# Kernel optimization log

Measured on AMD Instinct MI355X. Metric: run time of the kernel, lower is better.

Reference implementation:

```python
import jax, jax.numpy as jnp
import numpy as np

K = 3      # kernel size (fixed by 18 = 2*K*K offset channels)
PAD = 1
EPS = 1e-5 # BatchNorm eps


def setup_inputs() -> dict:
    key = jax.random.key(0)
    ks = jax.random.split(key, 4)
    B, Cin, Cout, H, W = 8, 64, 64, 96, 96
    x = jax.random.normal(ks[0], (B, Cin, H, W), jnp.float32)
    # small offset-conv weights so predicted offsets stay within a few pixels
    w_off = jax.random.normal(ks[1], (2 * K * K, Cin, K, K), jnp.float32) * 0.02
    b_off = jnp.zeros((2 * K * K,), jnp.float32)
    w_def = jax.random.normal(ks[2], (Cout, Cin, K, K), jnp.float32) * (1.0 / np.sqrt(Cin * K * K))
    b_def = jnp.zeros((Cout,), jnp.float32)
    gamma = jnp.ones((Cout,), jnp.float32)
    beta = jnp.zeros((Cout,), jnp.float32)
    return dict(x=x, w_off=w_off, b_off=b_off, w_def=w_def, b_def=b_def, gamma=gamma, beta=beta)


def _deform_sample(x, offset):
    """Bilinear-sample x at deformed kernel tap locations.
    x: (B,C,H,W); offset: (B,2*K*K,H,W) with (dy,dx) pairs per tap, row-major.
    Returns (B,C,K*K,H,W). Out-of-bounds samples are zero (torchvision semantics).
    """
    B, C, H, W = x.shape
    off = offset.reshape(B, K * K, 2, H, W)
    dy, dx = off[:, :, 0], off[:, :, 1]              # (B,9,H,W)
    ky = (jnp.arange(K * K) // K).astype(x.dtype)    # tap row index
    kx = (jnp.arange(K * K) % K).astype(x.dtype)     # tap col index
    base_y = jnp.arange(H, dtype=x.dtype)[:, None] - PAD   # (H,1)
    base_x = jnp.arange(W, dtype=x.dtype)[None, :] - PAD   # (1,W)
    py = dy + ky[None, :, None, None] + base_y[None, None]  # (B,9,H,W)
    px = dx + kx[None, :, None, None] + base_x[None, None]
    y0 = jnp.floor(py)
    x0 = jnp.floor(px)
    wy1 = py - y0
    wx1 = px - x0
    wy0 = 1.0 - wy1
    wx0 = 1.0 - wx1
    xflat = x.reshape(B, C, H * W)
    acc = jnp.zeros((B, C, K * K * H * W), x.dtype)
    corners = [(y0, x0, wy0 * wx0), (y0, x0 + 1.0, wy0 * wx1),
               (y0 + 1.0, x0, wy1 * wx0), (y0 + 1.0, x0 + 1.0, wy1 * wx1)]
    for yc, xc, wc in corners:
        valid = (yc >= 0) & (yc <= H - 1) & (xc >= 0) & (xc <= W - 1)
        iy = jnp.clip(yc, 0, H - 1).astype(jnp.int32)
        ix = jnp.clip(xc, 0, W - 1).astype(jnp.int32)
        idx = (iy * W + ix).reshape(B, 1, K * K * H * W)
        v = jnp.take_along_axis(xflat, idx, axis=2)          # (B,C,9HW) gather
        w = jnp.where(valid, wc, 0.0).reshape(B, 1, K * K * H * W)
        acc = acc + v * w
    return acc.reshape(B, C, K * K, H, W)


def reference(x, w_off, b_off, w_def, b_def, gamma, beta):
    # 1) offset-predicting conv
    offset = jax.lax.conv_general_dilated(
        x, w_off, window_strides=(1, 1), padding=((PAD, PAD), (PAD, PAD)),
        dimension_numbers=("NCHW", "OIHW", "NCHW")) + b_off[None, :, None, None]
    # 2) deformable conv: bilinear gather then per-pixel contraction over (C, taps)
    sampled = _deform_sample(x, offset)                      # (B,C,9,H,W)
    Cout = w_def.shape[0]
    y = jnp.einsum("bckhw,ock->bohw", sampled, w_def.reshape(Cout, -1, K * K))
    y = y + b_def[None, :, None, None]
    # 3) BatchNorm2d (training mode: batch statistics) + ReLU
    mean = y.mean(axis=(0, 2, 3))
    var = y.var(axis=(0, 2, 3))
    y = (y - mean[None, :, None, None]) * jax.lax.rsqrt(var[None, :, None, None] + EPS)
    y = gamma[None, :, None, None] * y + beta[None, :, None, None]
    return jax.nn.relu(y)
```

## Files before the change

kernel.cpp:

```cpp
#include <hip/hip_runtime.h>
#include <hip/hip_bf16.h>
#include <stdint.h>

static constexpr int NBATCH = 8;
static constexpr int Cin  = 64;
static constexpr int Cout = 64;
static constexpr int H = 96, W = 96;
static constexpr int HW   = H * W;
static constexpr int NPIX = NBATCH * HW;
static constexpr int NBLK = NPIX / 64;
static constexpr int BLK_PER_BATCH = HW / 64;
static constexpr float EPS = 1e-5f;

typedef short  bf16x8 __attribute__((ext_vector_type(8)));
typedef float  f32x4  __attribute__((ext_vector_type(4)));

__device__ inline uint16_t f2bf(float f) {
    __hip_bfloat16 h = __float2bfloat16(f);
    return *reinterpret_cast<uint16_t*>(&h);
}
__device__ inline float bf2f(uint16_t u) {
    union { uint32_t i; float f; } z;
    z.i = ((uint32_t)u) << 16;
    return z.f;
}
__device__ inline void gld_lds16(const void* g, void* l) {
    __builtin_amdgcn_global_load_lds(
        (const __attribute__((address_space(1))) void*)g,
        (__attribute__((address_space(3))) void*)l, 16, 0, 0);
}

__global__ void repack(const float* __restrict__ w_off,
                       const float* __restrict__ w_def,
                       uint16_t* __restrict__ woffPack,
                       uint16_t* __restrict__ wdefPack,
                       float* __restrict__ zeropage) {
    int t0 = blockIdx.x * blockDim.x + threadIdx.x;
    int stride = gridDim.x * blockDim.x;
    if (t0 < 64) zeropage[t0] = 0.f;
    for (int i = t0; i < 72 * 32 * 8; i += stride) {
        int e = i & 7;
        int n = (i >> 3) & 31;
        int sg = i >> 8;
        int k = sg * 8 + e;
        int tap = k >> 6, c = k & 63;
        woffPack[i] = (n < 18) ? f2bf(w_off[(n * Cin + c) * 9 + tap]) : (uint16_t)0;
    }
    for (int i = t0; i < 72 * 64 * 8; i += stride) {
        int e = i & 7;
        int n = (i >> 3) & 63;
        int sg = i >> 9;
        int k = sg * 8 + e;
        int tap = k >> 6, c = k & 63;
        wdefPack[i] = f2bf(w_def[(n * Cin + c) * 9 + tap]);
    }
}

__global__ __launch_bounds__(256) void transpose_x(const float* __restrict__ x,
                                                   uint16_t* __restrict__ xT) {
    int t = blockIdx.x * 256 + threadIdx.x;
    int pix  = t >> 1;
    int half = t & 1;
    int b = pix / HW, rem = pix % HW;
    const float* xb = x + (size_t)(b * Cin) * HW + rem + (size_t)(half * 32) * HW;
    uint16_t* o = xT + (size_t)pix * 64 + half * 32;
#pragma unroll
    for (int cg = 0; cg < 4; ++cg) {
        bf16x8 v;
#pragma unroll
        for (int e = 0; e < 8; ++e) v[e] = (short)f2bf(xb[(cg * 8 + e) * HW]);
        *reinterpret_cast<bf16x8*>(o + cg * 8) = v;
    }
}

__global__ __launch_bounds__(512, 4) void fused_deform(
        const uint16_t* __restrict__ xT,
        const uint16_t* __restrict__ woffPack,
        const uint16_t* __restrict__ wdefPack,
        const float* __restrict__ b_off,
        const float* __restrict__ zeropage,
        float* __restrict__ y,
        float* __restrict__ partial) {
    __shared__ __attribute__((aligned(16))) char smem[73728];
    __shared__ float offs[64 * 18];
    __shared__ float s_red[128];
    short* As   = (short*)smem;
    float* osum = (float*)smem;
    float* red  = (float*)smem;

    int tid  = threadIdx.x;
    int lane = tid & 63;
    int wv   = tid >> 6;
    int l15  = lane & 15;
    int lg   = lane >> 4;

    int wgid  = (blockIdx.x & 7) * BLK_PER_BATCH + (blockIdx.x >> 3);
    int gpix0 = wgid * 64;
    int b     = gpix0 / HW;
    int rem0  = gpix0 % HW;
    const uint16_t* xTb = xT + (size_t)b * HW * 64;

    int pr   = (wv << 3) + (lane >> 3);
    int e8   = lane & 7;
    int slot = e8 ^ (pr & 7);
    int remP = rem0 + pr;
    int hP   = remP / W, wP = remP % W;

    {
        const uint16_t* gsrc = xTb + slot * 8;
        char* ldsbase = (char*)As + (size_t)wv * 1024;
#pragma unroll
        for (int tap = 0; tap < 9; ++tap) {
            int yy = hP + tap / 3 - 1;
            int xx = wP + tap % 3 - 1;
            bool ok = (yy >= 0) && (yy < H) && (xx >= 0) && (xx < W);
            const void* g = ok ? (const void*)(gsrc + (yy * W + xx) * 64)
                               : (const void*)zeropage;
            gld_lds16(g, ldsbase + tap * 8192);
        }
    }
    __syncthreads();

    {
        int wj = wv & 1;
        int kq = wv >> 1;
        int sbeg = (kq < 2) ? kq * 5 : 2 + kq * 4;
        int send = (kq < 2) ? sbeg + 5 : sbeg + 4;
        f32x4 oacc[4];
#pragma unroll
        for (int m = 0; m < 4; ++m) oacc[m] = (f32x4){0.f, 0.f, 0.f, 0.f};
        for (int s = sbeg; s < send; ++s) {
            int sg = s * 4 + lg;
            bf16x8 bb = *reinterpret_cast<const bf16x8*>(
                woffPack + (sg * 32 + wj * 16 + l15) * 8);
#pragma unroll
            for (int m = 0; m < 4; ++m) {
                bf16x8 a = *reinterpret_cast<const bf16x8*>(
                    &As[(((sg >> 3) * 64 + m * 16 + l15) * 8 + ((sg & 7) ^ (l15 & 7))) * 8]);
                oacc[m] = __builtin_amdgcn_mfma_f32_16x16x32_bf16(a, bb, oacc[m], 0, 0, 0);
            }
        }
        __syncthreads();
#pragma unroll
        for (int m = 0; m < 4; ++m)
#pragma unroll
            for (int r = 0; r < 4; ++r)
                osum[(kq * 64 + m * 16 + lg * 4 + r) * 34 + wj * 16 + l15] = oacc[m][r];
        __syncthreads();
        for (int i = tid; i < 64 * 18; i += 512) {
            int rr = i / 18, o = i - rr * 18;
            offs[i] = osum[rr * 34 + o] + osum[(64 + rr) * 34 + o]
                    + osum[(128 + rr) * 34 + o] + osum[(192 + rr) * 34 + o] + b_off[o];
        }
        if (tid < 128) s_red[tid] = 0.f;
        __syncthreads();
    }

    {
        float hm1 = (float)(hP - 1), wm1 = (float)(wP - 1);
        float w00a, w01a, w10a, w11a; int i00a, i01a, i10a, i11a;
        {
            int t = e8;
            int ty = (t * 11) >> 5;
            int tx = t - 3 * ty;
            float dy = offs[pr * 18 + 2 * t];
            float dx = offs[pr * 18 + 2 * t + 1];
            float py = dy + (float)ty + hm1;
            float px = dx + (float)tx + wm1;
            float y0f = floorf(py), x0f = floorf(px);
            float wy1 = py - y0f, wx1 = px - x0f;
            float wy0 = 1.f - wy1, wx0 = 1.f - wx1;
            int iy0 = (int)y0f, ix0 = (int)x0f;
            int iy1 = iy0 + 1,  ix1 = ix0 + 1;
            bool vy0 = (iy0 >= 0) && (iy0 < H), vy1 = (iy1 >= 0) && (iy1 < H);
            bool vx0 = (ix0 >= 0) && (ix0 < W), vx1 = (ix1 >= 0) && (ix1 < W);
            w00a = (vy0 && vx0) ? wy0 * wx0 : 0.f;
            w01a = (vy0 && vx1) ? wy0 * wx1 : 0.f;
            w10a = (vy1 && vx0) ? wy1 * wx0 : 0.f;
            w11a = (vy1 && vx1) ? wy1 * wx1 : 0.f;
            int cy0 = min(max(iy0, 0), H - 1), cy1 = min(max(iy1, 0), H - 1);
            int cx0 = min(max(ix0, 0), W - 1), cx1 = min(max(ix1, 0), W - 1);
            i00a = cy0 * W + cx0; i01a = cy0 * W + cx1;
            i10a = cy1 * W + cx0; i11a = cy1 * W + cx1;
        }
        float w00b, w01b, w10b, w11b; int i00b, i01b, i10b, i11b;
        {
            float dy = offs[pr * 18 + 16];
            float dx = offs[pr * 18 + 17];
            float py = dy + 2.f + hm1;
            float px = dx + 2.f + wm1;
            float y0f = floorf(py), x0f = floorf(px);
            float wy1 = py - y0f, wx1 = px - x0f;
            float wy0 = 1.f - wy1, wx0 = 1.f - wx1;
            int iy0 = (int)y0f, ix0 = (int)x0f;
            int iy1 = iy0 + 1,  ix1 = ix0 + 1;
            bool vy0 = (iy0 >= 0) && (iy0 < H), vy1 = (iy1 >= 0) && (iy1 < H);
            bool vx0 = (ix0 >= 0) && (ix0 < W), vx1 = (ix1 >= 0) && (ix1 < W);
            w00b = (vy0 && vx0) ? wy0 * wx0 : 0.f;
            w01b = (vy0 && vx1) ? wy0 * wx1 : 0.f;
            w10b = (vy1 && vx0) ? wy1 * wx0 : 0.f;
            w11b = (vy1 && vx1) ? wy1 * wx1 : 0.f;
            int cy0 = min(max(iy0, 0), H - 1), cy1 = min(max(iy1, 0), H - 1);
            int cx0 = min(max(ix0, 0), W - 1), cx1 = min(max(ix1, 0), W - 1);
            i00b = cy0 * W + cx0; i01b = cy0 * W + cx1;
            i10b = cy1 * W + cx0; i11b = cy1 * W + cx1;
        }

        const uint16_t* basep = xTb + e8 * 8;
        int lanebase = lane & 56;
#pragma unroll
        for (int tap = 0; tap < 9; ++tap) {
            float w00, w01, w10, w11; int i00, i01, i10, i11;
            if (tap < 8) {
                int src = lanebase + tap;
                w00 = __shfl(w00a, src); w01 = __shfl(w01a, src);
                w10 = __shfl(w10a, src); w11 = __shfl(w11a, src);
                i00 = __shfl(i00a, src); i01 = __shfl(i01a, src);
                i10 = __shfl(i10a, src); i11 = __shfl(i11a, src);
            } else {
                w00 = w00b; w01 = w01b; w10 = w10b; w11 = w11b;
                i00 = i00b; i01 = i01b; i10 = i10b; i11 = i11b;
            }
            bf16x8 v00 = *reinterpret_cast<const bf16x8*>(basep + i00 * 64);
            bf16x8 v01 = *reinterpret_cast<const bf16x8*>(basep + i01 * 64);
            bf16x8 v10 = *reinterpret_cast<const bf16x8*>(basep + i10 * 64);
            bf16x8 v11 = *reinterpret_cast<const bf16x8*>(basep + i11 * 64);
            bf16x8 outv;
#pragma unroll
            for (int e = 0; e < 8; ++e) {
                float s = w00 * bf2f((uint16_t)v00[e]) + w01 * bf2f((uint16_t)v01[e])
                        + w10 * bf2f((uint16_t)v10[e]) + w11 * bf2f((uint16_t)v11[e]);
                outv[e] = (short)f2bf(s);
            }
            *reinterpret_cast<bf16x8*>(&As[((tap * 64 + pr) * 8 + slot) * 8]) = outv;
        }
    }
    __syncthreads();

    {
        int nf = wv & 3;
        int kh = wv >> 2;
        f32x4 acc[4];
#pragma unroll
        for (int m = 0; m < 4; ++m) acc[m] = (f32x4){0.f, 0.f, 0.f, 0.f};
#pragma unroll
        for (int s = 0; s < 9; ++s) {
            int sg = (kh * 9 + s) * 4 + lg;
            bf16x8 bb = *reinterpret_cast<const bf16x8*>(
                wdefPack + (sg * 64 + nf * 16 + l15) * 8);
#pragma unroll
            for (int m = 0; m < 4; ++m) {
                bf16x8 a = *reinterpret_cast<const bf16x8*>(
                    &As[(((sg >> 3) * 64 + m * 16 + l15) * 8 + ((sg & 7) ^ (l15 & 7))) * 8]);
                acc[m] = __builtin_amdgcn_mfma_f32_16x16x32_bf16(a, bb, acc[m], 0, 0, 0);
            }
        }
        __syncthreads();
#pragma unroll
        for (int m = 0; m < 4; ++m)
#pragma unroll
            for (int r = 0; r < 4; ++r)
                red[(kh * 64 + m * 16 + lg * 4 + r) * 66 + nf * 16 + l15] = acc[m][r];
        __syncthreads();

        int c  = lane;
        int rg = wv;
        f32x4 v0, v1;
        float s = 0.f, q = 0.f;
#pragma unroll
        for (int k2 = 0; k2 < 8; ++k2) {
            int r = rg * 8 + k2;
            float v = red[r * 66 + c] + red[(64 + r) * 66 + c];
            if (k2 < 4) v0[k2] = v; else v1[k2 - 4] = v;
            s += v; q += v * v;
        }
        float* yp = y + ((size_t)b * Cout + c) * HW + rem0 + rg * 8;
        *reinterpret_cast<f32x4*>(yp)     = v0;
        *reinterpret_cast<f32x4*>(yp + 4) = v1;
        atomicAdd(&s_red[c], s);
        atomicAdd(&s_red[64 + c], q);
    }
    __syncthreads();
    if (tid < 128) partial[(size_t)wgid * 128 + tid] = s_red[tid];
}

__global__ __launch_bounds__(256) void bn_reduce1(const float* __restrict__ partial,
                                                  float* __restrict__ partial2) {
    __shared__ float red[256];
    int ch = threadIdx.x & 127;
    int g  = threadIdx.x >> 7;
    float s = 0.f;
#pragma unroll
    for (int r = 0; r < 8; ++r)
        s += partial[(size_t)(blockIdx.x * 16 + g * 8 + r) * 128 + ch];
    red[threadIdx.x] = s;
    __syncthreads();
    if (g == 0)
        partial2[(size_t)blockIdx.x * 128 + ch] = red[ch] + red[128 + ch];
}

__global__ void bn_stats2(const float* __restrict__ partial2,
                          const float* __restrict__ gamma,
                          const float* __restrict__ beta,
                          float* __restrict__ stats) {
    __shared__ float red[256];
    int ch = threadIdx.x & 127;
    int g  = threadIdx.x >> 7;
    float s = 0.f;
    for (int i = 0; i < 36; ++i)
        s += partial2[(size_t)(g * 36 + i) * 128 + ch];
    red[threadIdx.x] = s;
    __syncthreads();
    if (threadIdx.x < 64) {
        int c = threadIdx.x;
        float sum = red[c] + red[128 + c];
        float sq  = red[64 + c] + red[192 + c];
        float mean = sum / (float)NPIX;
        float var  = sq / (float)NPIX - mean * mean;
        float v    = var + EPS;
        float inv  = rsqrtf(v);
        inv = inv * (1.5f - 0.5f * v * inv * inv);
        float sc = gamma[c] * inv;
        stats[c]      = sc;
        stats[64 + c] = beta[c] - mean * sc;
    }
}

__global__ __launch_bounds__(256) void bn_apply(float* __restrict__ y,
                                                const float* __restrict__ stats) {
    int t = blockIdx.x * blockDim.x + threadIdx.x;
    int e = t * 4;
    int ch = (e / HW) % Cout;
    float sc = stats[ch];
    float sh = stats[64 + ch];
    float4 v = *reinterpret_cast<float4*>(y + e);
    v.x = fmaxf(v.x * sc + sh, 0.f);
    v.y = fmaxf(v.y * sc + sh, 0.f);
    v.z = fmaxf(v.z * sc + sh, 0.f);
    v.w = fmaxf(v.w * sc + sh, 0.f);
    *reinterpret_cast<float4*>(y + e) = v;
}

extern "C" void kernel_launch(void* const* d_in, const int* in_sizes, int n_in,
                              void* d_out, int out_size, void* d_ws, size_t ws_size,
                              hipStream_t stream) {
    const float* x     = (const float*)d_in[0];
    const float* w_off = (const float*)d_in[1];
    const float* b_off = (const float*)d_in[2];
    const float* w_def = (const float*)d_in[3];
    const float* gamma = (const float*)d_in[5];
    const float* beta  = (const float*)d_in[6];
    float* out = (float*)d_out;
    char*  ws  = (char*)d_ws;

    uint16_t* xT       = (uint16_t*)ws;
    uint16_t* woffPack = (uint16_t*)(ws + 9437184);
    uint16_t* wdefPack = (uint16_t*)(ws + 9474048);
    float*    partial  = (float*)(ws + 9547776);
    float*    partial2 = (float*)(ws + 10137600);
    float*    stats    = (float*)(ws + 10174464);
    float*    zeropage = (float*)(ws + 10174976);

    repack<<<64, 256, 0, stream>>>(w_off, w_def, woffPack, wdefPack, zeropage);
    transpose_x<<<NPIX * 2 / 256, 256, 0, stream>>>(x, xT);
    fused_deform<<<NBLK, 512, 0, stream>>>(xT, woffPack, wdefPack, b_off,
                                           zeropage, out, partial);
    bn_reduce1<<<72, 256, 0, stream>>>(partial, partial2);
    bn_stats2<<<1, 256, 0, stream>>>(partial2, gamma, beta, stats);
    bn_apply<<<(NPIX * Cout / 4) / 256, 256, 0, stream>>>(out, stats);
}
```

Measured before the change: 67.08 us.

## Store pre-BN output as bf16, software-pipeline bilinear gathers, raise MFMA wave priority

The pre-BatchNorm conv output now goes to a bf16 workspace buffer, and bn_apply reads bf16 and writes fp32 to the output. This roughly halves the intermediate write and re-read traffic. The 9-tap bilinear gather loop is manually double-buffered so the loads for tap t+1 are issued before tap t is blended. s_setprio raises wave priority around both MFMA loops. The risk is extra rounding error from storing y in bf16 before normalization.

```diff
diff --git a/kernel.cpp b/kernel.cpp
--- a/kernel.cpp
+++ b/kernel.cpp
@@ -73,13 +73,45 @@
     }
 }
 
+#define P3_SETUP(T, W00,W01,W10,W11,I00,I01,I10,I11)                        \
+    if ((T) < 8) {                                                          \
+        int src_ = lanebase + (T);                                          \
+        W00 = __shfl(w00a, src_); W01 = __shfl(w01a, src_);                 \
+        W10 = __shfl(w10a, src_); W11 = __shfl(w11a, src_);                 \
+        I00 = __shfl(i00a, src_); I01 = __shfl(i01a, src_);                 \
+        I10 = __shfl(i10a, src_); I11 = __shfl(i11a, src_);                 \
+    } else {                                                                \
+        W00 = w00b; W01 = w01b; W10 = w10b; W11 = w11b;                     \
+        I00 = i00b; I01 = i01b; I10 = i10b; I11 = i11b;                     \
+    }
+
+#define P3_ISSUE(I00,I01,I10,I11,C00,C01,C10,C11)                           \
+    C00 = *reinterpret_cast<const bf16x8*>(basep + (I00) * 64);             \
+    C01 = *reinterpret_cast<const bf16x8*>(basep + (I01) * 64);             \
+    C10 = *reinterpret_cast<const bf16x8*>(basep + (I10) * 64);             \
+    C11 = *reinterpret_cast<const bf16x8*>(basep + (I11) * 64);
+
+#define P3_CONV(T, W00,W01,W10,W11,C00,C01,C10,C11)                         \
+    {                                                                       \
+        bf16x8 outv_;                                                       \
+        _Pragma("unroll")                                                   \
+        for (int e = 0; e < 8; ++e) {                                       \
+            float s_ = (W00) * bf2f((uint16_t)(C00)[e])                     \
+                     + (W01) * bf2f((uint16_t)(C01)[e])                     \
+                     + (W10) * bf2f((uint16_t)(C10)[e])                     \
+                     + (W11) * bf2f((uint16_t)(C11)[e]);                    \
+            outv_[e] = (short)f2bf(s_);                                     \
+        }                                                                   \
+        *reinterpret_cast<bf16x8*>(&As[(((T) * 64 + pr) * 8 + slot) * 8]) = outv_; \
+    }
+
 __global__ __launch_bounds__(512, 4) void fused_deform(
         const uint16_t* __restrict__ xT,
         const uint16_t* __restrict__ woffPack,
         const uint16_t* __restrict__ wdefPack,
         const float* __restrict__ b_off,
         const float* __restrict__ zeropage,
-        float* __restrict__ y,
+        uint16_t* __restrict__ ybf,
         float* __restrict__ partial) {
     __shared__ __attribute__((aligned(16))) char smem[73728];
     __shared__ float offs[64 * 18];
@@ -129,6 +161,7 @@
         f32x4 oacc[4];
 #pragma unroll
         for (int m = 0; m < 4; ++m) oacc[m] = (f32x4){0.f, 0.f, 0.f, 0.f};
+        __builtin_amdgcn_s_setprio(1);
         for (int s = sbeg; s < send; ++s) {
             int sg = s * 4 + lg;
             bf16x8 bb = *reinterpret_cast<const bf16x8*>(
@@ -140,6 +173,7 @@
                 oacc[m] = __builtin_amdgcn_mfma_f32_16x16x32_bf16(a, bb, oacc[m], 0, 0, 0);
             }
         }
+        __builtin_amdgcn_s_setprio(0);
         __syncthreads();
 #pragma unroll
         for (int m = 0; m < 4; ++m)
@@ -208,32 +242,37 @@
 
         const uint16_t* basep = xTb + e8 * 8;
         int lanebase = lane & 56;
-#pragma unroll
-        for (int tap = 0; tap < 9; ++tap) {
-            float w00, w01, w10, w11; int i00, i01, i10, i11;
-            if (tap < 8) {
-                int src = lanebase + tap;
-                w00 = __shfl(w00a, src); w01 = __shfl(w01a, src);
-                w10 = __shfl(w10a, src); w11 = __shfl(w11a, src);
-                i00 = __shfl(i00a, src); i01 = __shfl(i01a, src);
-                i10 = __shfl(i10a, src); i11 = __shfl(i11a, src);
-            } else {
-                w00 = w00b; w01 = w01b; w10 = w10b; w11 = w11b;
-                i00 = i00b; i01 = i01b; i10 = i10b; i11 = i11b;
-            }
-            bf16x8 v00 = *reinterpret_cast<const bf16x8*>(basep + i00 * 64);
-            bf16x8 v01 = *reinterpret_cast<const bf16x8*>(basep + i01 * 64);
-            bf16x8 v10 = *reinterpret_cast<const bf16x8*>(basep + i10 * 64);
-            bf16x8 v11 = *reinterpret_cast<const bf16x8*>(basep + i11 * 64);
-            bf16x8 outv;
-#pragma unroll
-            for (int e = 0; e < 8; ++e) {
-                float s = w00 * bf2f((uint16_t)v00[e]) + w01 * bf2f((uint16_t)v01[e])
-                        + w10 * bf2f((uint16_t)v10[e]) + w11 * bf2f((uint16_t)v11[e]);
-                outv[e] = (short)f2bf(s);
-            }
-            *reinterpret_cast<bf16x8*>(&As[((tap * 64 + pr) * 8 + slot) * 8]) = outv;
-        }
+
+        float uA0,uA1,uA2,uA3; int jA0,jA1,jA2,jA3; bf16x8 cA0,cA1,cA2,cA3;
+        float uB0,uB1,uB2,uB3; int jB0,jB1,jB2,jB3; bf16x8 cB0,cB1,cB2,cB3;
+
+        P3_SETUP(0, uA0,uA1,uA2,uA3, jA0,jA1,jA2,jA3)
+        P3_ISSUE(jA0,jA1,jA2,jA3, cA0,cA1,cA2,cA3)
+        P3_SETUP(1, uB0,uB1,uB2,uB3, jB0,jB1,jB2,jB3)
+        P3_ISSUE(jB0,jB1,jB2,jB3, cB0,cB1,cB2,cB3)
+        P3_CONV(0, uA0,uA1,uA2,uA3, cA0,cA1,cA2,cA3)
+        P3_SETUP(2, uA0,uA1,uA2,uA3, jA0,jA1,jA2,jA3)
+        P3_ISSUE(jA0,jA1,jA2,jA3, cA0,cA1,cA2,cA3)
+        P3_CONV(1, uB0,uB1,uB2,uB3, cB0,cB1,cB2,cB3)
+        P3_SETUP(3, uB0,uB1,uB2,uB3, jB0,jB1,jB2,jB3)
+        P3_ISSUE(jB0,jB1,jB2,jB3, cB0,cB1,cB2,cB3)
+        P3_CONV(2, uA0,uA1,uA2,uA3, cA0,cA1,cA2,cA3)
+        P3_SETUP(4, uA0,uA1,uA2,uA3, jA0,jA1,jA2,jA3)
+        P3_ISSUE(jA0,jA1,jA2,jA3, cA0,cA1,cA2,cA3)
+        P3_CONV(3, uB0,uB1,uB2,uB3, cB0,cB1,cB2,cB3)
+        P3_SETUP(5, uB0,uB1,uB2,uB3, jB0,jB1,jB2,jB3)
+        P3_ISSUE(jB0,jB1,jB2,jB3, cB0,cB1,cB2,cB3)
+        P3_CONV(4, uA0,uA1,uA2,uA3, cA0,cA1,cA2,cA3)
+        P3_SETUP(6, uA0,uA1,uA2,uA3, jA0,jA1,jA2,jA3)
+        P3_ISSUE(jA0,jA1,jA2,jA3, cA0,cA1,cA2,cA3)
+        P3_CONV(5, uB0,uB1,uB2,uB3, cB0,cB1,cB2,cB3)
+        P3_SETUP(7, uB0,uB1,uB2,uB3, jB0,jB1,jB2,jB3)
+        P3_ISSUE(jB0,jB1,jB2,jB3, cB0,cB1,cB2,cB3)
+        P3_CONV(6, uA0,uA1,uA2,uA3, cA0,cA1,cA2,cA3)
+        P3_SETUP(8, uA0,uA1,uA2,uA3, jA0,jA1,jA2,jA3)
+        P3_ISSUE(jA0,jA1,jA2,jA3, cA0,cA1,cA2,cA3)
+        P3_CONV(7, uB0,uB1,uB2,uB3, cB0,cB1,cB2,cB3)
+        P3_CONV(8, uA0,uA1,uA2,uA3, cA0,cA1,cA2,cA3)
     }
     __syncthreads();
 
@@ -243,6 +282,7 @@
         f32x4 acc[4];
 #pragma unroll
         for (int m = 0; m < 4; ++m) acc[m] = (f32x4){0.f, 0.f, 0.f, 0.f};
+        __builtin_amdgcn_s_setprio(1);
 #pragma unroll
         for (int s = 0; s < 9; ++s) {
             int sg = (kh * 9 + s) * 4 + lg;
@@ -255,6 +295,7 @@
                 acc[m] = __builtin_amdgcn_mfma_f32_16x16x32_bf16(a, bb, acc[m], 0, 0, 0);
             }
         }
+        __builtin_amdgcn_s_setprio(0);
         __syncthreads();
 #pragma unroll
         for (int m = 0; m < 4; ++m)
@@ -265,18 +306,17 @@
 
         int c  = lane;
         int rg = wv;
-        f32x4 v0, v1;
+        bf16x8 ov;
         float s = 0.f, q = 0.f;
 #pragma unroll
         for (int k2 = 0; k2 < 8; ++k2) {
             int r = rg * 8 + k2;
             float v = red[r * 66 + c] + red[(64 + r) * 66 + c];
-            if (k2 < 4) v0[k2] = v; else v1[k2 - 4] = v;
+            ov[k2] = (short)f2bf(v);
             s += v; q += v * v;
         }
-        float* yp = y + ((size_t)b * Cout + c) * HW + rem0 + rg * 8;
-        *reinterpret_cast<f32x4*>(yp)     = v0;
-        *reinterpret_cast<f32x4*>(yp + 4) = v1;
+        *reinterpret_cast<bf16x8*>(
+            ybf + ((size_t)b * Cout + c) * HW + rem0 + rg * 8) = ov;
         atomicAdd(&s_red[c], s);
         atomicAdd(&s_red[64 + c], q);
     }
@@ -326,19 +366,23 @@
     }
 }
 
-__global__ __launch_bounds__(256) void bn_apply(float* __restrict__ y,
+__global__ __launch_bounds__(256) void bn_apply(const uint16_t* __restrict__ ybf,
+                                                float* __restrict__ out,
                                                 const float* __restrict__ stats) {
     int t = blockIdx.x * blockDim.x + threadIdx.x;
-    int e = t * 4;
-    int ch = (e / HW) % Cout;
+    int e = t * 8;
+    int ch = (e / HW) & 63;
     float sc = stats[ch];
     float sh = stats[64 + ch];
-    float4 v = *reinterpret_cast<float4*>(y + e);
-    v.x = fmaxf(v.x * sc + sh, 0.f);
-    v.y = fmaxf(v.y * sc + sh, 0.f);
-    v.z = fmaxf(v.z * sc + sh, 0.f);
-    v.w = fmaxf(v.w * sc + sh, 0.f);
-    *reinterpret_cast<float4*>(y + e) = v;
+    bf16x8 v = *reinterpret_cast<const bf16x8*>(ybf + e);
+    f32x4 o0, o1;
+#pragma unroll
+    for (int i = 0; i < 4; ++i) {
+        o0[i] = fmaxf(bf2f((uint16_t)v[i])     * sc + sh, 0.f);
+        o1[i] = fmaxf(bf2f((uint16_t)v[4 + i]) * sc + sh, 0.f);
+    }
+    *reinterpret_cast<f32x4*>(out + e)     = o0;
+    *reinterpret_cast<f32x4*>(out + e + 4) = o1;
 }
 
 extern "C" void kernel_launch(void* const* d_in, const int* in_sizes, int n_in,
@@ -360,12 +404,13 @@
     float*    partial2 = (float*)(ws + 10137600);
     float*    stats    = (float*)(ws + 10174464);
     float*    zeropage = (float*)(ws + 10174976);
+    uint16_t* ybf      = (uint16_t*)(ws + 10175232);
 
     repack<<<64, 256, 0, stream>>>(w_off, w_def, woffPack, wdefPack, zeropage);
     transpose_x<<<NPIX * 2 / 256, 256, 0, stream>>>(x, xT);
     fused_deform<<<NBLK, 512, 0, stream>>>(xT, woffPack, wdefPack, b_off,
-                                           zeropage, out, partial);
+                                           zeropage, ybf, partial);
     bn_reduce1<<<72, 256, 0, stream>>>(partial, partial2);
     bn_stats2<<<1, 256, 0, stream>>>(partial2, gamma, beta, stats);
-    bn_apply<<<(NPIX * Cout / 4) / 256, 256, 0, stream>>>(out, stats);
-}
+    bn_apply<<<(NPIX * Cout / 8) / 256, 256, 0, stream>>>(ybf, out, stats);
+}
```

New measurement: 65.99 us. No clear change (-1.6%).
